# Kernel optimization log

Hardware: AMD Instinct MI355X
Metric: run time of the kernel (lower is better)

## Reference

```python
import jax, jax.numpy as jnp
import numpy as np

B, F, N = 8, 2048, 10000   # batch, features_dim, n_tiles
J, R = 10, 20
H1, H2 = 200, 100


def setup_inputs() -> dict:
    key = jax.random.key(0)
    ks = jax.random.split(key, 8)
    s = lambda fan_in: 1.0 / np.sqrt(fan_in)
    return {
        "x": jax.random.normal(ks[0], (B, F, N), dtype=jnp.float32),
        "conv_w": jax.random.uniform(ks[1], (J, F), jnp.float32, -s(F), s(F)),
        "conv_b": jax.random.uniform(ks[2], (J,), jnp.float32, -s(F), s(F)),
        "w1": jax.random.uniform(ks[3], (2 * R * J, H1), jnp.float32, -s(2 * R * J), s(2 * R * J)),
        "b1": jnp.zeros((H1,), jnp.float32),
        "w2": jax.random.uniform(ks[4], (H1, H2), jnp.float32, -s(H1), s(H1)),
        "b2": jnp.zeros((H2,), jnp.float32),
        "w3": jax.random.uniform(ks[5], (H2, 2), jnp.float32, -s(H2), s(H2)),
        "b3": jnp.zeros((2,), jnp.float32),
    }


def reference(x, conv_w, conv_b, w1, b1, w2, b2, w3, b3):
    # 1x1 Conv1d: [B,F,N] x [J,F] -> [B,J,N]
    emb = jnp.einsum("bfn,jf->bjn", x, conv_w) + conv_b[None, :, None]
    # MinMax: top-R (descending) and bottom-R (also in descending order,
    # matching the tail of a descending full sort).
    top_vals, _ = jax.lax.top_k(emb, R)                    # [B,J,R] descending
    neg_bot, _ = jax.lax.top_k(-emb, R)                    # smallest R, ascending in value
    bot_vals = jnp.flip(-neg_bot, axis=2)                  # [B,J,R] descending
    mm = jnp.concatenate([top_vals, bot_vals], axis=2)     # [B,J,2R]
    h = mm.reshape(mm.shape[0], -1)                        # [B, 2*R*J]
    h = jax.nn.sigmoid(h @ w1 + b1)
    h = jax.nn.sigmoid(h @ w2 + b2)
    return h @ w3 + b3                                     # [B, 2] logits
```

## Files before the change

kernel.cpp:

```cpp
#include <hip/hip_runtime.h>
#include <math.h>
#include <float.h>

#define B_   8
#define F_   2048
#define N_   10000
#define J_   10
#define R_   20
#define H1_  200
#define H2_  100

#define FC_     16
#define FCHUNK  (F_ / FC_)
#define VN      4
#define T1      256
#define NPB     (T1 * VN)
#define NB      ((N_ + NPB - 1) / NPB)
#define PLANE   ((size_t)B_ * J_ * N_)

__global__ __launch_bounds__(T1) void conv_kernel(
    const float* __restrict__ x, const float* __restrict__ w,
    float* __restrict__ part)
{
    const int tid = threadIdx.x;
    const int nb  = blockIdx.x;
    const int b   = blockIdx.y;
    const int fc  = blockIdx.z;

    const int n0 = nb * NPB + tid * VN;
    if (n0 >= N_) return;
    const int fbeg = fc * FCHUNK;

    const float* px = x + ((size_t)b * F_ + fbeg) * N_ + n0;
    const float* pw = w + fbeg;

    float4 acc[J_];
#pragma unroll
    for (int j = 0; j < J_; ++j) acc[j] = make_float4(0.f, 0.f, 0.f, 0.f);

#pragma unroll 2
    for (int f = 0; f < FCHUNK; ++f) {
        const float4 xv = *(const float4*)px;
        px += N_;
#pragma unroll
        for (int j = 0; j < J_; ++j) {
            const float wv = pw[j * F_ + f];
            acc[j].x = fmaf(wv, xv.x, acc[j].x);
            acc[j].y = fmaf(wv, xv.y, acc[j].y);
            acc[j].z = fmaf(wv, xv.z, acc[j].z);
            acc[j].w = fmaf(wv, xv.w, acc[j].w);
        }
    }

    float* pe = part + (size_t)fc * PLANE + ((size_t)b * J_) * N_ + n0;
#pragma unroll
    for (int j = 0; j < J_; ++j) {
        *(float4*)(pe + (size_t)j * N_) = acc[j];
    }
}

#define T2  256
#define LPT 20

__global__ __launch_bounds__(T2) void select_kernel(
    const float* __restrict__ part, const float* __restrict__ conv_b,
    float* __restrict__ mm)
{
    __shared__ float ls_top[T2 * LPT];
    __shared__ float ls_bot[T2 * LPT];
    __shared__ float s_val[8];
    __shared__ int   s_tid[8];
    __shared__ float s_wv;
    __shared__ int   s_wt;

    const int tid = threadIdx.x;
    const int j   = blockIdx.x;
    const int b   = blockIdx.y;

    const float* row = part + ((size_t)b * J_ + j) * N_;

    float top[LPT], bot[LPT];
#pragma unroll
    for (int k = 0; k < LPT; ++k) { top[k] = -FLT_MAX; bot[k] = FLT_MAX; }

    for (int n = tid; n < N_; n += T2) {
        float v = 0.f;
#pragma unroll
        for (int fc = 0; fc < FC_; ++fc) v += row[(size_t)fc * PLANE + n];

        float tv = v;
#pragma unroll
        for (int k = 0; k < LPT; ++k) {
            if (tv > top[k]) { const float o = top[k]; top[k] = tv; tv = o; }
        }
        float bv = v;
#pragma unroll
        for (int k = 0; k < LPT; ++k) {
            if (bv < bot[k]) { const float o = bot[k]; bot[k] = bv; bv = o; }
        }
    }
#pragma unroll
    for (int k = 0; k < LPT; ++k) {
        ls_top[tid * LPT + k] = top[k];
        ls_bot[tid * LPT + k] = bot[k];
    }
    __syncthreads();

    const float bias = conv_b[j];
    float* out = mm + ((size_t)b * J_ + j) * (2 * R_);

    const int lane = tid & 63;
    const int wv_  = tid >> 6;
    int ht = 0, hb = 0;

    for (int r = 0; r < R_; ++r) {
        {
            float v = ls_top[tid * LPT + ht];
            int   t = tid;
            for (int off = 32; off; off >>= 1) {
                const float vo = __shfl_down(v, off);
                const int   to = __shfl_down(t, off);
                if (vo > v) { v = vo; t = to; }
            }
            if (lane == 0) { s_val[wv_] = v; s_tid[wv_] = t; }
            __syncthreads();
            if (tid == 0) {
                float bv2 = s_val[0]; int bt = s_tid[0];
                for (int q = 1; q < T2 / 64; ++q)
                    if (s_val[q] > bv2) { bv2 = s_val[q]; bt = s_tid[q]; }
                s_wv = bv2; s_wt = bt;
            }
            __syncthreads();
            if (tid == s_wt) { ht++; out[r] = s_wv + bias; }
            __syncthreads();
        }
        {
            float v = ls_bot[tid * LPT + hb];
            int   t = tid;
            for (int off = 32; off; off >>= 1) {
                const float vo = __shfl_down(v, off);
                const int   to = __shfl_down(t, off);
                if (vo < v) { v = vo; t = to; }
            }
            if (lane == 0) { s_val[wv_] = v; s_tid[wv_] = t; }
            __syncthreads();
            if (tid == 0) {
                float bv2 = s_val[0]; int bt = s_tid[0];
                for (int q = 1; q < T2 / 64; ++q)
                    if (s_val[q] < bv2) { bv2 = s_val[q]; bt = s_tid[q]; }
                s_wv = bv2; s_wt = bt;
            }
            __syncthreads();
            if (tid == s_wt) { hb++; out[2 * R_ - 1 - r] = s_wv + bias; }
            __syncthreads();
        }
    }
}

__global__ __launch_bounds__(256) void mlp_kernel(
    const float* __restrict__ mm,
    const float* __restrict__ w1, const float* __restrict__ b1,
    const float* __restrict__ w2, const float* __restrict__ b2,
    const float* __restrict__ w3, const float* __restrict__ b3,
    float* __restrict__ out)
{
    __shared__ float h0[2 * R_ * J_];
    __shared__ float h1[H1_];
    __shared__ float h2[H2_];

    const int tid = threadIdx.x;
    const int b   = blockIdx.x;

    for (int i = tid; i < 2 * R_ * J_; i += 256) h0[i] = mm[b * 2 * R_ * J_ + i];
    __syncthreads();

    if (tid < H1_) {
        float acc = b1[tid];
#pragma unroll 4
        for (int i = 0; i < 2 * R_ * J_; ++i)
            acc = fmaf(h0[i], w1[i * H1_ + tid], acc);
        h1[tid] = 1.f / (1.f + expf(-acc));
    }
    __syncthreads();

    if (tid < H2_) {
        float acc = b2[tid];
#pragma unroll 4
        for (int i = 0; i < H1_; ++i)
            acc = fmaf(h1[i], w2[i * H2_ + tid], acc);
        h2[tid] = 1.f / (1.f + expf(-acc));
    }
    __syncthreads();

    if (tid < 2) {
        float acc = b3[tid];
        for (int i = 0; i < H2_; ++i)
            acc = fmaf(h2[i], w3[i * 2 + tid], acc);
        out[b * 2 + tid] = acc;
    }
}

extern "C" void kernel_launch(void* const* d_in, const int* in_sizes, int n_in,
                              void* d_out, int out_size, void* d_ws, size_t ws_size,
                              hipStream_t stream)
{
    const float* x      = (const float*)d_in[0];
    const float* conv_w = (const float*)d_in[1];
    const float* conv_b = (const float*)d_in[2];
    const float* w1     = (const float*)d_in[3];
    const float* b1     = (const float*)d_in[4];
    const float* w2     = (const float*)d_in[5];
    const float* b2     = (const float*)d_in[6];
    const float* w3     = (const float*)d_in[7];
    const float* b3     = (const float*)d_in[8];

    float* part = (float*)d_ws;
    float* mm   = part + (size_t)FC_ * PLANE;
    float* out  = (float*)d_out;

    conv_kernel<<<dim3(NB, B_, FC_), T1, 0, stream>>>(x, conv_w, part);
    select_kernel<<<dim3(J_, B_), T2, 0, stream>>>(part, conv_b, mm);
    mlp_kernel<<<B_, 256, 0, stream>>>(mm, w1, b1, w2, b2, w3, b3, out);
}
```

Before: 958.6 us.

## Reduce F split in-block via shared memory instead of global partial planes

```diff
diff --git a/kernel.cpp b/kernel.cpp
--- a/kernel.cpp
+++ b/kernel.cpp
@@ -10,52 +10,58 @@
 #define H1_  200
 #define H2_  100
 
-#define FC_     16
-#define FCHUNK  (F_ / FC_)
-#define VN      4
-#define T1      256
-#define NPB     (T1 * VN)
-#define NB      ((N_ + NPB - 1) / NPB)
-#define PLANE   ((size_t)B_ * J_ * N_)
+#define T1     256
+#define NBLK   128
+#define NB     ((N_ + NBLK - 1) / NBLK)
+#define FSLICE (F_ / 4)
 
 __global__ __launch_bounds__(T1) void conv_kernel(
     const float* __restrict__ x, const float* __restrict__ w,
-    float* __restrict__ part)
-{
-    const int tid = threadIdx.x;
-    const int nb  = blockIdx.x;
-    const int b   = blockIdx.y;
-    const int fc  = blockIdx.z;
-
-    const int n0 = nb * NPB + tid * VN;
-    if (n0 >= N_) return;
-    const int fbeg = fc * FCHUNK;
-
-    const float* px = x + ((size_t)b * F_ + fbeg) * N_ + n0;
-    const float* pw = w + fbeg;
-
-    float4 acc[J_];
-#pragma unroll
-    for (int j = 0; j < J_; ++j) acc[j] = make_float4(0.f, 0.f, 0.f, 0.f);
-
-#pragma unroll 2
-    for (int f = 0; f < FCHUNK; ++f) {
-        const float4 xv = *(const float4*)px;
+    float* __restrict__ emb)
+{
+    __shared__ float ls[4][J_][NBLK];
+
+    const int tid  = threadIdx.x;
+    const int wid  = tid >> 6;
+    const int lane = tid & 63;
+    const int b    = blockIdx.y;
+
+    int n0 = blockIdx.x * NBLK;
+    if (n0 > N_ - NBLK) n0 = N_ - NBLK;
+    const int n  = n0 + 2 * lane;
+    const int f0 = wid * FSLICE;
+
+    const float* px = x + ((size_t)b * F_ + f0) * N_ + n;
+    const float* pw = w + f0;
+
+    float2 acc[J_];
+#pragma unroll
+    for (int j = 0; j < J_; ++j) acc[j] = make_float2(0.f, 0.f);
+
+#pragma unroll 4
+    for (int f = 0; f < FSLICE; ++f) {
+        const float2 xv = *(const float2*)px;
         px += N_;
 #pragma unroll
         for (int j = 0; j < J_; ++j) {
-            const float wv = pw[j * F_ + f];
-            acc[j].x = fmaf(wv, xv.x, acc[j].x);
-            acc[j].y = fmaf(wv, xv.y, acc[j].y);
-            acc[j].z = fmaf(wv, xv.z, acc[j].z);
-            acc[j].w = fmaf(wv, xv.w, acc[j].w);
-        }
-    }
-
-    float* pe = part + (size_t)fc * PLANE + ((size_t)b * J_) * N_ + n0;
-#pragma unroll
-    for (int j = 0; j < J_; ++j) {
-        *(float4*)(pe + (size_t)j * N_) = acc[j];
+            const float wj = pw[j * F_ + f];
+            acc[j].x = fmaf(wj, xv.x, acc[j].x);
+            acc[j].y = fmaf(wj, xv.y, acc[j].y);
+        }
+    }
+
+#pragma unroll
+    for (int j = 0; j < J_; ++j)
+        *(float2*)&ls[wid][j][2 * lane] = acc[j];
+    __syncthreads();
+
+#pragma unroll
+    for (int k = 0; k < 5; ++k) {
+        const int idx = tid + k * 256;
+        const int j   = idx >> 7;
+        const int nl  = idx & (NBLK - 1);
+        const float v = ls[0][j][nl] + ls[1][j][nl] + ls[2][j][nl] + ls[3][j][nl];
+        emb[((size_t)b * J_ + j) * N_ + n0 + nl] = v;
     }
 }
 
@@ -63,7 +69,7 @@
 #define LPT 20
 
 __global__ __launch_bounds__(T2) void select_kernel(
-    const float* __restrict__ part, const float* __restrict__ conv_b,
+    const float* __restrict__ emb, const float* __restrict__ conv_b,
     float* __restrict__ mm)
 {
     __shared__ float ls_top[T2 * LPT];
@@ -77,16 +83,14 @@
     const int j   = blockIdx.x;
     const int b   = blockIdx.y;
 
-    const float* row = part + ((size_t)b * J_ + j) * N_;
+    const float* row = emb + ((size_t)b * J_ + j) * N_;
 
     float top[LPT], bot[LPT];
 #pragma unroll
     for (int k = 0; k < LPT; ++k) { top[k] = -FLT_MAX; bot[k] = FLT_MAX; }
 
     for (int n = tid; n < N_; n += T2) {
-        float v = 0.f;
-#pragma unroll
-        for (int fc = 0; fc < FC_; ++fc) v += row[(size_t)fc * PLANE + n];
+        const float v = row[n];
 
         float tv = v;
 #pragma unroll
@@ -214,11 +218,11 @@
     const float* w3     = (const float*)d_in[7];
     const float* b3     = (const float*)d_in[8];
 
-    float* part = (float*)d_ws;
-    float* mm   = part + (size_t)FC_ * PLANE;
-    float* out  = (float*)d_out;
-
-    conv_kernel<<<dim3(NB, B_, FC_), T1, 0, stream>>>(x, conv_w, part);
-    select_kernel<<<dim3(J_, B_), T2, 0, stream>>>(part, conv_b, mm);
+    float* emb = (float*)d_ws;
+    float* mm  = emb + (size_t)B_ * J_ * N_;
+    float* out = (float*)d_out;
+
+    conv_kernel<<<dim3(NB, B_), T1, 0, stream>>>(x, conv_w, emb);
+    select_kernel<<<dim3(J_, B_), T2, 0, stream>>>(emb, conv_b, mm);
     mlp_kernel<<<B_, 256, 0, stream>>>(mm, w1, b1, w2, b2, w3, b3, out);
 }
```

Measured after the change: 1.047 ms. 9.3% more time.
